# Kernel optimization log

Measured on AMD Instinct MI355X. Metric: run time of the kernel, lower is better.

## Reference

```python
import jax, jax.numpy as jnp
import numpy as np

B, TD, TE, V, D, DFF, L, H = 16, 256, 1024, 5000, 512, 2048, 6, 8

def setup_inputs():
    key = jax.random.key(0)
    ks = jax.random.split(key, 32)
    s = 0.02
    def w(k, shape):
        return jax.random.normal(k, shape, jnp.float32) * s
    # targets drawn in [3, V) so the eos filter in the torch code is a no-op
    inp = {
        "targets": jax.random.randint(ks[0], (B, TD), 3, V),
        "target_lengths": jax.random.randint(ks[1], (B,), TD // 2, TD + 1),
        "encoder_outputs": jax.random.normal(ks[2], (B, TE, D), jnp.float32),
        "encoder_output_lengths": jax.random.randint(ks[3], (B,), TE // 2, TE + 1),
        "emb": w(ks[4], (V, D)),
        "W_in": w(ks[5], (D, D)), "b_in": jnp.zeros((D,), jnp.float32),
        "ln1_g": jnp.ones((L, D), jnp.float32), "ln1_b": jnp.zeros((L, D), jnp.float32),
        "Wq1": w(ks[6], (L, D, D)), "bq1": jnp.zeros((L, D), jnp.float32),
        "Wk1": w(ks[7], (L, D, D)), "bk1": jnp.zeros((L, D), jnp.float32),
        "Wv1": w(ks[8], (L, D, D)), "bv1": jnp.zeros((L, D), jnp.float32),
        "Wo1": w(ks[9], (L, D, D)), "bo1": jnp.zeros((L, D), jnp.float32),
        "ln2_g": jnp.ones((L, D), jnp.float32), "ln2_b": jnp.zeros((L, D), jnp.float32),
        "Wq2": w(ks[10], (L, D, D)), "bq2": jnp.zeros((L, D), jnp.float32),
        "Wk2": w(ks[11], (L, D, D)), "bk2": jnp.zeros((L, D), jnp.float32),
        "Wv2": w(ks[12], (L, D, D)), "bv2": jnp.zeros((L, D), jnp.float32),
        "Wo2": w(ks[13], (L, D, D)), "bo2": jnp.zeros((L, D), jnp.float32),
        "ln3_g": jnp.ones((L, D), jnp.float32), "ln3_b": jnp.zeros((L, D), jnp.float32),
        "W_ff1": w(ks[14], (L, D, DFF)), "b_ff1": jnp.zeros((L, DFF), jnp.float32),
        "W_ff2": w(ks[15], (L, DFF, D)), "b_ff2": jnp.zeros((L, D), jnp.float32),
    }
    return inp

def _ln(x, g, b, eps=1e-5):
    m = x.mean(-1, keepdims=True)
    v = ((x - m) ** 2).mean(-1, keepdims=True)
    return (x - m) * jax.lax.rsqrt(v + eps) * g + b

def _mha(q, k, v, Wq, bq, Wk, bk, Wv, bv, Wo, bo, mask):
    Bq, Tq, Dm = q.shape
    dh = Dm // H
    def heads(x, W, bias):
        y = x @ W + bias
        return y.reshape(x.shape[0], x.shape[1], H, dh).transpose(0, 2, 1, 3)  # (B,H,T,dh)
    qh, kh, vh = heads(q, Wq, bq), heads(k, Wk, bk), heads(v, Wv, bv)
    sc = jnp.einsum('bhqd,bhkd->bhqk', qh, kh) / jnp.sqrt(jnp.float32(dh))
    sc = jnp.where(mask[:, None, :, :], jnp.float32(-1e9), sc)
    a = jax.nn.softmax(sc, axis=-1)
    ctx = jnp.einsum('bhqk,bhkd->bhqd', a, vh).transpose(0, 2, 1, 3).reshape(Bq, Tq, Dm)
    return ctx @ Wo + bo

def _pos_encoding(length, dim):
    pos = jnp.arange(length, dtype=jnp.float32)[:, None]
    div = jnp.exp(jnp.arange(0, dim, 2, dtype=jnp.float32) * (-jnp.log(jnp.float32(10000.0)) / dim))
    pe = jnp.zeros((length, dim), jnp.float32)
    pe = pe.at[:, 0::2].set(jnp.sin(pos * div)).at[:, 1::2].set(jnp.cos(pos * div))
    return pe

def _forward(targets, target_lengths, encoder_output_lengths, encoder_outputs, emb, W_in, b_in, ln1_g, ln1_b, Wq1, bq1, Wk1, bk1, Wv1, bv1, Wo1, bo1, ln2_g, ln2_b, Wq2, bq2, Wk2, bk2, Wv2, bv2, Wo2, bo2, ln3_g, ln3_b, W_ff1, b_ff1, W_ff2, b_ff2):
    Bsz, Td = targets.shape
    Te = encoder_outputs.shape[1]
    key_pad = jnp.arange(Td)[None, :] >= target_lengths[:, None]            # (B, Td) pad keys
    causal = jnp.triu(jnp.ones((Td, Td), bool), k=1)                        # subsequent mask
    self_mask = key_pad[:, None, :] | causal[None]                          # (B, Td, Td)
    enc_pad = jnp.arange(Te)[None, :] >= encoder_output_lengths[:, None]    # (B, Te)
    enc_mask = jnp.broadcast_to(enc_pad[:, None, :], (Bsz, Td, Te))
    # TransformerEmbedding: lookup * sqrt(dim), then sinusoidal PE, then input_proj
    x = emb[targets] * jnp.sqrt(jnp.float32(D)) + _pos_encoding(Td, D)[None]
    x = x @ W_in + b_in
    for l in range(L):  # pre-LN decoder layers: self-attn, cross-attn, FFN
        h = _ln(x, ln1_g[l], ln1_b[l])
        x = x + _mha(h, h, h, Wq1[l], bq1[l], Wk1[l], bk1[l], Wv1[l], bv1[l], Wo1[l], bo1[l], self_mask)
        h = _ln(x, ln2_g[l], ln2_b[l])
        x = x + _mha(h, encoder_outputs, encoder_outputs, Wq2[l], bq2[l], Wk2[l], bk2[l], Wv2[l], bv2[l], Wo2[l], bo2[l], enc_mask)
        h = _ln(x, ln3_g[l], ln3_b[l])
        x = x + (jax.nn.relu(h @ W_ff1[l] + b_ff1[l]) @ W_ff2[l] + b_ff2[l])
    # torch code stacks step_outputs[:, di, :] over di, i.e. returns the hidden states (B, Td, D)
    return x

def reference(targets, target_lengths, encoder_outputs, encoder_output_lengths, emb, W_in, b_in, ln1_g, ln1_b, Wq1, bq1, Wk1, bk1, Wv1, bv1, Wo1, bo1, ln2_g, ln2_b, Wq2, bq2, Wk2, bk2, Wv2, bv2, Wo2, bo2, ln3_g, ln3_b, W_ff1, b_ff1, W_ff2, b_ff2):
    return _forward(targets, target_lengths, encoder_output_lengths, encoder_outputs, emb, W_in, b_in, ln1_g, ln1_b, Wq1, bq1, Wk1, bk1, Wv1, bv1, Wo1, bo1, ln2_g, ln2_b, Wq2, bq2, Wk2, bk2, Wv2, bv2, Wo2, bo2, ln3_g, ln3_b, W_ff1, b_ff1, W_ff2, b_ff2)
```

## Files before the change

### kernel.cpp

```cpp
#include <hip/hip_runtime.h>
#include <hip/hip_bf16.h>

#define BB   16
#define TD   256
#define TE   1024
#define DM   512
#define DFF  2048
#define NL   6
#define NH   8
#define DH   64

typedef unsigned short u16;
typedef short short8 __attribute__((ext_vector_type(8)));
typedef float f32x4 __attribute__((ext_vector_type(4)));

__device__ __forceinline__ float b2f(u16 u) {
    unsigned int x = ((unsigned int)u) << 16;
    float f;
    __builtin_memcpy(&f, &x, 4);
    return f;
}
__device__ __forceinline__ u16 f2b(float f) {
    unsigned int x;
    __builtin_memcpy(&x, &f, 4);
    unsigned int r = x + 0x7fffu + ((x >> 16) & 1u);
    return (u16)(r >> 16);
}

__device__ __forceinline__ void gload_lds16(const u16* g, u16* l) {
    __builtin_amdgcn_global_load_lds(
        (const __attribute__((address_space(1))) unsigned int*)g,
        (__attribute__((address_space(3))) unsigned int*)l, 16, 0, 0);
}

__global__ __launch_bounds__(256) void cvt_kernel(const float* __restrict__ in,
                                                  u16* __restrict__ out, int n4) {
    int i = blockIdx.x * 256 + threadIdx.x;
    if (i < n4) {
        float4 v = reinterpret_cast<const float4*>(in)[i];
        ushort4 o;
        o.x = f2b(v.x); o.y = f2b(v.y); o.z = f2b(v.z); o.w = f2b(v.w);
        reinterpret_cast<ushort4*>(out)[i] = o;
    }
}

template <int NMAT>
struct PtrArr { const float* p[NMAT]; };

template <int NMAT>
__global__ __launch_bounds__(256) void tr_kernel(PtrArr<NMAT> P, u16* __restrict__ out,
                                                 int K, int N) {
    __shared__ u16 t[64][65];
    const float* W = P.p[blockIdx.z];
    u16* O = out + (size_t)blockIdx.z * K * N;
    int n0 = blockIdx.x * 64, k0 = blockIdx.y * 64;
    int tid = threadIdx.x;
    int r = tid >> 4, c = (tid & 15) * 4;
#pragma unroll
    for (int p = 0; p < 4; ++p) {
        int k = r + p * 16;
        float4 v = *reinterpret_cast<const float4*>(&W[(size_t)(k0 + k) * N + n0 + c]);
        t[c + 0][k] = f2b(v.x);
        t[c + 1][k] = f2b(v.y);
        t[c + 2][k] = f2b(v.z);
        t[c + 3][k] = f2b(v.w);
    }
    __syncthreads();
#pragma unroll
    for (int p = 0; p < 4; ++p) {
        int n = r + p * 16;
        ushort4 o;
        o.x = t[n][c]; o.y = t[n][c + 1]; o.z = t[n][c + 2]; o.w = t[n][c + 3];
        *reinterpret_cast<ushort4*>(&O[(size_t)(n0 + n) * K + k0 + c]) = o;
    }
}

__global__ __launch_bounds__(256) void embed_kernel(const int* __restrict__ targets,
                                                    const float* __restrict__ emb,
                                                    u16* __restrict__ out) {
    int row = blockIdx.x;
    int t   = row & (TD - 1);
    int tgt = targets[row];
    const float c = -0.017988946039015984f;
    for (int d = threadIdx.x; d < DM; d += 256) {
        float e   = emb[(size_t)tgt * DM + d] * 22.627416997969522f;
        int   i2  = d & ~1;
        float div = expf(c * (float)i2);
        float arg = (float)t * div;
        float pe  = (d & 1) ? cosf(arg) : sinf(arg);
        out[(size_t)row * DM + d] = f2b(e + pe);
    }
}

__global__ __launch_bounds__(256) void ln_kernel(const float* __restrict__ X,
                                                 const float* __restrict__ g,
                                                 const float* __restrict__ b,
                                                 size_t vo,
                                                 u16* __restrict__ O) {
    int row = blockIdx.x;
    const float* xr = X + (size_t)row * DM;
    int tid = threadIdx.x;
    float v0 = xr[tid], v1 = xr[tid + 256];
    float s = v0 + v1;
    __shared__ float red[4];
    int lane = tid & 63, wid = tid >> 6;
#pragma unroll
    for (int off = 32; off; off >>= 1) s += __shfl_xor(s, off);
    if (lane == 0) red[wid] = s;
    __syncthreads();
    float mean = (red[0] + red[1] + red[2] + red[3]) * (1.0f / 512.0f);
    float d0 = v0 - mean, d1 = v1 - mean;
    float sq = d0 * d0 + d1 * d1;
#pragma unroll
    for (int off = 32; off; off >>= 1) sq += __shfl_xor(sq, off);
    __syncthreads();
    if (lane == 0) red[wid] = sq;
    __syncthreads();
    float var = (red[0] + red[1] + red[2] + red[3]) * (1.0f / 512.0f);
    float rs  = rsqrtf(var + 1e-5f);
    O[(size_t)row * DM + tid]       = f2b(d0 * rs * g[vo + tid]       + b[vo + tid]);
    O[(size_t)row * DM + tid + 256] = f2b(d1 * rs * g[vo + tid + 256] + b[vo + tid + 256]);
}

template <int TM, int TN, bool OUTBF, bool RELU, bool RES>
__global__ __launch_bounds__(256) void gemm_bt(const u16* __restrict__ A,
                                               const u16* __restrict__ Bt,
                                               const float* __restrict__ bias, size_t bofs,
                                               const float* __restrict__ resid,
                                               void* __restrict__ C,
                                               int M, int N, int K) {
    __shared__ u16 As[2][TM * 32];
    __shared__ u16 Bs[2][TN * 32];
    int tid = threadIdx.x, wave = tid >> 6, lane = tid & 63;
    int col0 = blockIdx.x * TN, row0 = blockIdx.y * TM;
    constexpr int WM = TM / 2, WN = TN / 2;
    int wm = (wave >> 1) * WM, wn = (wave & 1) * WN;
    int lq = lane >> 4, lc = lane & 15;
    constexpr int NI = WM / 16, NJ = WN / 16;
    f32x4 acc[NI][NJ] = {};
    int srow = lane >> 2;
    int scol = (lane & 3) * 8;

    auto stage = [&](int buf, int k0) {
#pragma unroll
        for (int s = 0; s < TM / 64; ++s) {
            int rbase = wave * (TM / 4) + s * 16;
            gload_lds16(A + (size_t)(row0 + rbase + srow) * K + k0 + scol, &As[buf][rbase * 32]);
        }
#pragma unroll
        for (int s = 0; s < TN / 64; ++s) {
            int rbase = wave * (TN / 4) + s * 16;
            gload_lds16(Bt + (size_t)(col0 + rbase + srow) * K + k0 + scol, &Bs[buf][rbase * 32]);
        }
    };

    stage(0, 0);
    __syncthreads();
    int cur = 0;
    for (int k0 = 0; k0 < K; k0 += 32) {
        if (k0 + 32 < K) stage(cur ^ 1, k0 + 32);
        short8 af[NI], bf[NJ];
#pragma unroll
        for (int i = 0; i < NI; ++i)
            af[i] = *reinterpret_cast<const short8*>(&As[cur][(wm + i * 16 + lc) * 32 + lq * 8]);
#pragma unroll
        for (int j = 0; j < NJ; ++j)
            bf[j] = *reinterpret_cast<const short8*>(&Bs[cur][(wn + j * 16 + lc) * 32 + lq * 8]);
#pragma unroll
        for (int i = 0; i < NI; ++i)
#pragma unroll
            for (int j = 0; j < NJ; ++j)
                acc[i][j] = __builtin_amdgcn_mfma_f32_16x16x32_bf16(af[i], bf[j], acc[i][j], 0, 0, 0);
        __syncthreads();
        cur ^= 1;
    }

#pragma unroll
    for (int j = 0; j < NJ; ++j) {
        int n = col0 + wn + j * 16 + lc;
        float bv = bias[bofs + n];
#pragma unroll
        for (int i = 0; i < NI; ++i) {
#pragma unroll
            for (int r = 0; r < 4; ++r) {
                int m = row0 + wm + i * 16 + lq * 4 + r;
                float v = acc[i][j][r] + bv;
                if (RES)  v += resid[(size_t)m * N + n];
                if (RELU) v = fmaxf(v, 0.0f);
                if (OUTBF) ((u16*)C)[(size_t)m * N + n] = f2b(v);
                else       ((float*)C)[(size_t)m * N + n] = v;
            }
        }
    }
}

template <int NG>
struct MOut { u16* out[NG]; const float* bias[NG]; };

template <int TM, int TN, int NG>
__global__ __launch_bounds__(256) void gemm_bt_multi(const u16* __restrict__ A,
                                                     const u16* __restrict__ Bt,
                                                     MOut<NG> mo, int K) {
    __shared__ u16 As[2][TM * 32];
    __shared__ u16 Bs[2][TN * 32];
    int tid = threadIdx.x, wave = tid >> 6, lane = tid & 63;
    int col0 = blockIdx.x * TN, row0 = blockIdx.y * TM;
    constexpr int WM = TM / 2, WN = TN / 2;
    int wm = (wave >> 1) * WM, wn = (wave & 1) * WN;
    int lq = lane >> 4, lc = lane & 15;
    constexpr int NI = WM / 16, NJ = WN / 16;
    f32x4 acc[NI][NJ] = {};
    int srow = lane >> 2;
    int scol = (lane & 3) * 8;

    auto stage = [&](int buf, int k0) {
#pragma unroll
        for (int s = 0; s < TM / 64; ++s) {
            int rbase = wave * (TM / 4) + s * 16;
            gload_lds16(A + (size_t)(row0 + rbase + srow) * K + k0 + scol, &As[buf][rbase * 32]);
        }
#pragma unroll
        for (int s = 0; s < TN / 64; ++s) {
            int rbase = wave * (TN / 4) + s * 16;
            gload_lds16(Bt + (size_t)(col0 + rbase + srow) * K + k0 + scol, &Bs[buf][rbase * 32]);
        }
    };

    stage(0, 0);
    __syncthreads();
    int cur = 0;
    for (int k0 = 0; k0 < K; k0 += 32) {
        if (k0 + 32 < K) stage(cur ^ 1, k0 + 32);
        short8 af[NI], bf[NJ];
#pragma unroll
        for (int i = 0; i < NI; ++i)
            af[i] = *reinterpret_cast<const short8*>(&As[cur][(wm + i * 16 + lc) * 32 + lq * 8]);
#pragma unroll
        for (int j = 0; j < NJ; ++j)
            bf[j] = *reinterpret_cast<const short8*>(&Bs[cur][(wn + j * 16 + lc) * 32 + lq * 8]);
#pragma unroll
        for (int i = 0; i < NI; ++i)
#pragma unroll
            for (int j = 0; j < NJ; ++j)
                acc[i][j] = __builtin_amdgcn_mfma_f32_16x16x32_bf16(af[i], bf[j], acc[i][j], 0, 0, 0);
        __syncthreads();
        cur ^= 1;
    }

    int g  = col0 >> 9;
    int c0 = col0 & 511;
    u16* O = mo.out[g];
    const float* bp = mo.bias[g];
#pragma unroll
    for (int j = 0; j < NJ; ++j) {
        int n = c0 + wn + j * 16 + lc;
        float bv = bp[n];
#pragma unroll
        for (int i = 0; i < NI; ++i) {
#pragma unroll
            for (int r = 0; r < 4; ++r) {
                int m = row0 + wm + i * 16 + lq * 4 + r;
                O[(size_t)m * 512 + n] = f2b(acc[i][j][r] + bv);
            }
        }
    }
}

#define QSTR 72
#define VSTR 66

__global__ __launch_bounds__(256) void fattn_mfma(const u16* __restrict__ Q,
                                                  const u16* __restrict__ K,
                                                  const u16* __restrict__ V,
                                                  const int* __restrict__ lens,
                                                  u16* __restrict__ O,
                                                  int Tq, int Tk, int causal) {
    __shared__ u16 Qs[64 * QSTR];
    __shared__ u16 Ks[64 * QSTR];
    __shared__ u16 Ps[64 * QSTR];
    __shared__ u16 Vs[64 * VSTR];
    int tid  = threadIdx.x;
    int qt0  = blockIdx.x * 64;
    int h    = blockIdx.y;
    int b    = blockIdx.z;
    int len  = lens[b];
    int wave = tid >> 6, lane = tid & 63;
    int lq = lane >> 4, lc = lane & 15;
    int sr = tid >> 4;
    int sd = (tid & 15) * 4;

    short8 bones;
    {
        u16 v = (lc == 0) ? (u16)0x3F80 : (u16)0;
        u16 tmp[8] = { v, v, v, v, v, v, v, v };
        __builtin_memcpy(&bones, tmp, 16);
    }

#pragma unroll
    for (int i = 0; i < 4; ++i) {
        int q = sr + i * 16;
        ushort4 v = *reinterpret_cast<const ushort4*>(
            &Q[(size_t)(b * Tq + qt0 + q) * DM + h * DH + sd]);
        ushort4 w;
        w.x = f2b(b2f(v.x) * 0.125f); w.y = f2b(b2f(v.y) * 0.125f);
        w.z = f2b(b2f(v.z) * 0.125f); w.w = f2b(b2f(v.w) * 0.125f);
        *reinterpret_cast<ushort4*>(&Qs[q * QSTR + sd]) = w;
    }

    ushort4 kr[4], vr[4];
#pragma unroll
    for (int i = 0; i < 4; ++i) {
        int k = sr + i * 16;
        kr[i] = *reinterpret_cast<const ushort4*>(&K[(size_t)(b * Tk + k) * DM + h * DH + sd]);
        vr[i] = *reinterpret_cast<const ushort4*>(&V[(size_t)(b * Tk + k) * DM + h * DH + sd]);
    }
#pragma unroll
    for (int i = 0; i < 4; ++i) {
        int k = sr + i * 16;
        *reinterpret_cast<ushort4*>(&Ks[k * QSTR + sd]) = kr[i];
        Vs[(sd + 0) * VSTR + k] = vr[i].x;
        Vs[(sd + 1) * VSTR + k] = vr[i].y;
        Vs[(sd + 2) * VSTR + k] = vr[i].z;
        Vs[(sd + 3) * VSTR + k] = vr[i].w;
    }
    __syncthreads();

    short8 aq0 = *reinterpret_cast<const short8*>(&Qs[(wave * 16 + lc) * QSTR + lq * 8]);
    short8 aq1 = *reinterpret_cast<const short8*>(&Qs[(wave * 16 + lc) * QSTR + 32 + lq * 8]);

    f32x4 Ow[4] = {};
    f32x4 Ol = {};

    int kend = causal ? min(len, qt0 + 64) : len;
    for (int kt0 = 0; kt0 < kend; kt0 += 64) {
        bool more = (kt0 + 64) < kend;
        if (more) {
#pragma unroll
            for (int i = 0; i < 4; ++i) {
                int k = kt0 + 64 + sr + i * 16;
                kr[i] = *reinterpret_cast<const ushort4*>(
                    &K[(size_t)(b * Tk + k) * DM + h * DH + sd]);
                vr[i] = *reinterpret_cast<const ushort4*>(
                    &V[(size_t)(b * Tk + k) * DM + h * DH + sd]);
            }
        }

        f32x4 sa[4] = {};
#pragma unroll
        for (int n = 0; n < 4; ++n) {
            short8 bk0 = *reinterpret_cast<const short8*>(&Ks[(n * 16 + lc) * QSTR + lq * 8]);
            short8 bk1 = *reinterpret_cast<const short8*>(&Ks[(n * 16 + lc) * QSTR + 32 + lq * 8]);
            sa[n] = __builtin_amdgcn_mfma_f32_16x16x32_bf16(aq0, bk0, sa[n], 0, 0, 0);
            sa[n] = __builtin_amdgcn_mfma_f32_16x16x32_bf16(aq1, bk1, sa[n], 0, 0, 0);
        }

        int qrow_base = qt0 + wave * 16 + lq * 4;
#pragma unroll
        for (int r = 0; r < 4; ++r) {
            int qrow = qrow_base + r;
#pragma unroll
            for (int n = 0; n < 4; ++n) {
                int key = kt0 + n * 16 + lc;
                bool inv = (key >= len) || (causal && key > qrow);
                float p = inv ? 0.0f : __expf(sa[n][r] - 8.0f);
                Ps[(wave * 16 + lq * 4 + r) * QSTR + n * 16 + lc] = f2b(p);
            }
        }

        short8 ap0 = *reinterpret_cast<const short8*>(&Ps[(wave * 16 + lc) * QSTR + lq * 8]);
        short8 ap1 = *reinterpret_cast<const short8*>(&Ps[(wave * 16 + lc) * QSTR + 32 + lq * 8]);
#pragma unroll
        for (int n = 0; n < 4; ++n) {
#pragma unroll
            for (int ks = 0; ks < 2; ++ks) {
                int base = (n * 16 + lc) * VSTR + ks * 32 + lq * 8;
                const int* vp = reinterpret_cast<const int*>(&Vs[base]);
                int w[4] = { vp[0], vp[1], vp[2], vp[3] };
                short8 bv;
                __builtin_memcpy(&bv, w, 16);
                Ow[n] = __builtin_amdgcn_mfma_f32_16x16x32_bf16(ks ? ap1 : ap0, bv, Ow[n], 0, 0, 0);
            }
        }
        Ol = __builtin_amdgcn_mfma_f32_16x16x32_bf16(ap0, bones, Ol, 0, 0, 0);
        Ol = __builtin_amdgcn_mfma_f32_16x16x32_bf16(ap1, bones, Ol, 0, 0, 0);

        __syncthreads();
        if (more) {
#pragma unroll
            for (int i = 0; i < 4; ++i) {
                int k = sr + i * 16;
                *reinterpret_cast<ushort4*>(&Ks[k * QSTR + sd]) = kr[i];
                Vs[(sd + 0) * VSTR + k] = vr[i].x;
                Vs[(sd + 1) * VSTR + k] = vr[i].y;
                Vs[(sd + 2) * VSTR + k] = vr[i].z;
                Vs[(sd + 3) * VSTR + k] = vr[i].w;
            }
            __syncthreads();
        }
    }

#pragma unroll
    for (int r = 0; r < 4; ++r) {
        float lsum = __shfl(Ol[r], lane & 48);
        float inv = 1.0f / lsum;
        size_t rowoff = (size_t)(b * Tq + qt0 + wave * 16 + lq * 4 + r) * DM + h * DH;
#pragma unroll
        for (int n = 0; n < 4; ++n)
            O[rowoff + n * 16 + lc] = f2b(Ow[n][r] * inv);
    }
}

__global__ __launch_bounds__(256) void store_out_kernel(const float* __restrict__ X,
                                                        float* __restrict__ out, int n) {
    int i = blockIdx.x * 256 + threadIdx.x;
    if (i < n) out[i] = X[i];
}

extern "C" void kernel_launch(void* const* d_in, const int* in_sizes, int n_in,
                              void* d_out, int out_size, void* d_ws, size_t ws_size,
                              hipStream_t stream) {
    const int*   targets = (const int*)d_in[0];
    const int*   tlen    = (const int*)d_in[1];
    const float* enc     = (const float*)d_in[2];
    const int*   elen    = (const int*)d_in[3];
    const float* emb     = (const float*)d_in[4];
    const float* W_in    = (const float*)d_in[5];
    const float* b_in    = (const float*)d_in[6];
    const float* ln1_g   = (const float*)d_in[7];
    const float* ln1_b   = (const float*)d_in[8];
    const float* Wq1 = (const float*)d_in[9],  *bq1 = (const float*)d_in[10];
    const float* Wk1 = (const float*)d_in[11], *bk1 = (const float*)d_in[12];
    const float* Wv1 = (const float*)d_in[13], *bv1 = (const float*)d_in[14];
    const float* Wo1 = (const float*)d_in[15], *bo1 = (const float*)d_in[16];
    const float* ln2_g = (const float*)d_in[17], *ln2_b = (const float*)d_in[18];
    const float* Wq2 = (const float*)d_in[19], *bq2 = (const float*)d_in[20];
    const float* Wk2 = (const float*)d_in[21], *bk2 = (const float*)d_in[22];
    const float* Wv2 = (const float*)d_in[23], *bv2 = (const float*)d_in[24];
    const float* Wo2 = (const float*)d_in[25], *bo2 = (const float*)d_in[26];
    const float* ln3_g = (const float*)d_in[27], *ln3_b = (const float*)d_in[28];
    const float* W_ff1 = (const float*)d_in[29], *b_ff1 = (const float*)d_in[30];
    const float* W_ff2 = (const float*)d_in[31], *b_ff2 = (const float*)d_in[32];

    float* ws   = (float*)d_ws;
    float* x    = ws;
    u16*   hb   = (u16*)(ws + 2097152);
    u16*   qb   = (u16*)(ws + 3145728);
    u16*   ctx  = (u16*)(ws + 4194304);
    u16*   kb   = (u16*)(ws + 5242880);
    u16*   vb   = (u16*)(ws + 9437184);
    u16*   encb = (u16*)(ws + 13631488);
    u16*   wt_dm = (u16*)(ws + 17825792);
    u16*   wt_f1 = (u16*)(ws + 24248320);
    u16*   wt_f2 = (u16*)(ws + 27394048);
    u16*   ffh  = kb;

    PtrArr<49> pdm;
    pdm.p[0] = W_in;
    for (int l = 0; l < NL; ++l) {
        const float* ws8[8] = { Wq1, Wk1, Wv1, Wo1, Wq2, Wk2, Wv2, Wo2 };
        for (int j = 0; j < 8; ++j) pdm.p[1 + l * 8 + j] = ws8[j] + (size_t)l * DM * DM;
    }
    PtrArr<6> pf1, pf2;
    for (int l = 0; l < NL; ++l) {
        pf1.p[l] = W_ff1 + (size_t)l * DM * DFF;
        pf2.p[l] = W_ff2 + (size_t)l * DFF * DM;
    }
    tr_kernel<49><<<dim3(8, 8, 49), 256, 0, stream>>>(pdm, wt_dm, 512, 512);
    tr_kernel<6><<<dim3(32, 8, 6), 256, 0, stream>>>(pf1, wt_f1, 512, 2048);
    tr_kernel<6><<<dim3(8, 32, 6), 256, 0, stream>>>(pf2, wt_f2, 2048, 512);

    const size_t WDM = (size_t)512 * 512;
    const size_t WFF = (size_t)512 * 2048;

    const dim3 gdm(8, 64);
    const dim3 gqkv(24, 64);
    const dim3 gkv2(8, 128);
    const dim3 gf1(16, 32);
    const dim3 gattn(TD / 64, NH, BB);

    cvt_kernel<<<8192, 256, 0, stream>>>(enc, encb, BB * TE * DM / 4);
    embed_kernel<<<4096, 256, 0, stream>>>(targets, emb, hb);
    gemm_bt<64, 64, false, false, false><<<gdm, 256, 0, stream>>>(hb, wt_dm, b_in, 0, nullptr, x, 4096, 512, 512);

    for (int l = 0; l < NL; ++l) {
        const size_t vo = (size_t)l * DM;
        const size_t fv = (size_t)l * DFF;
        const u16* tq1 = wt_dm + (1 + l * 8 + 0) * WDM;
        const u16* to1 = wt_dm + (1 + l * 8 + 3) * WDM;
        const u16* tq2 = wt_dm + (1 + l * 8 + 4) * WDM;
        const u16* tk2 = wt_dm + (1 + l * 8 + 5) * WDM;
        const u16* to2 = wt_dm + (1 + l * 8 + 7) * WDM;
        const u16* tf1 = wt_f1 + l * WFF;
        const u16* tf2 = wt_f2 + l * WFF;

        ln_kernel<<<4096, 256, 0, stream>>>(x, ln1_g, ln1_b, vo, hb);
        {
            MOut<3> mo;
            mo.out[0] = qb; mo.out[1] = kb; mo.out[2] = vb;
            mo.bias[0] = bq1 + vo; mo.bias[1] = bk1 + vo; mo.bias[2] = bv1 + vo;
            gemm_bt_multi<64, 64, 3><<<gqkv, 256, 0, stream>>>(hb, tq1, mo, 512);
        }
        fattn_mfma<<<gattn, 256, 0, stream>>>(qb, kb, vb, tlen, ctx, TD, TD, 1);
        gemm_bt<64, 64, false, false, true><<<gdm, 256, 0, stream>>>(ctx, to1, bo1, vo, x, x, 4096, 512, 512);

        ln_kernel<<<4096, 256, 0, stream>>>(x, ln2_g, ln2_b, vo, hb);
        gemm_bt<64, 64, true, false, false><<<gdm, 256, 0, stream>>>(hb, tq2, bq2, vo, nullptr, qb, 4096, 512, 512);
        {
            MOut<2> mo;
            mo.out[0] = kb; mo.out[1] = vb;
            mo.bias[0] = bk2 + vo; mo.bias[1] = bv2 + vo;
            gemm_bt_multi<128, 128, 2><<<gkv2, 256, 0, stream>>>(encb, tk2, mo, 512);
        }
        fattn_mfma<<<gattn, 256, 0, stream>>>(qb, kb, vb, elen, ctx, TD, TE, 0);
        gemm_bt<64, 64, false, false, true><<<gdm, 256, 0, stream>>>(ctx, to2, bo2, vo, x, x, 4096, 512, 512);

        ln_kernel<<<4096, 256, 0, stream>>>(x, ln3_g, ln3_b, vo, hb);
        gemm_bt<128, 128, true, true, false><<<gf1, 256, 0, stream>>>(hb, tf1, b_ff1, fv, nullptr, ffh, 4096, 2048, 512);
        gemm_bt<64, 64, false, false, true><<<gdm, 256, 0, stream>>>(ffh, tf2, b_ff2, vo, x, x, 4096, 512, 2048);
    }

    store_out_kernel<<<8192, 256, 0, stream>>>(x, (float*)d_out, BB * TD * DM);
}
```

Measured before the change: 1.361 ms.

## Split cross-attention over key halves, skip padded encoder K/V rows, retile GEMMs

Cross-attention now runs as two blocks per batch, each covering half of the 1024 encoder keys. Each half writes unnormalized partial outputs and row sums, and a new combine kernel merges them. Skipping the max-subtraction with a fixed exp offset is what makes this merge valid. The encoder K/V projection skips row tiles beyond each sequence's rounded-up encoder length, and the DM-sized GEMMs move from 64x64 to 128x64 or 128x128 tiles. This buys more attention parallelism and less wasted projection work, at the cost of an extra kernel launch, partial-result memory traffic, and fewer blocks in the retiled GEMMs.

Result: slower. 1.452 ms (+6.7%).

```diff
diff --git a/kernel.cpp b/kernel.cpp
--- a/kernel.cpp
+++ b/kernel.cpp
@@ -200,11 +200,21 @@
 template <int TM, int TN, int NG>
 __global__ __launch_bounds__(256) void gemm_bt_multi(const u16* __restrict__ A,
                                                      const u16* __restrict__ Bt,
-                                                     MOut<NG> mo, int K) {
+                                                     MOut<NG> mo, int K,
+                                                     const int* __restrict__ lens,
+                                                     int rbShift) {
     __shared__ u16 As[2][TM * 32];
     __shared__ u16 Bs[2][TN * 32];
     int tid = threadIdx.x, wave = tid >> 6, lane = tid & 63;
     int col0 = blockIdx.x * TN, row0 = blockIdx.y * TM;
+
+    if (lens) {
+        int bb  = row0 >> rbShift;
+        int rl  = row0 & ((1 << rbShift) - 1);
+        int lim = (lens[bb] + 63) & ~63;
+        if (rl >= lim) return;
+    }
+
     constexpr int WM = TM / 2, WN = TN / 2;
     int wm = (wave >> 1) * WM, wn = (wave & 1) * WN;
     int lq = lane >> 4, lc = lane & 15;
@@ -269,11 +279,14 @@
 #define QSTR 72
 #define VSTR 66
 
+template <bool SPLIT>
 __global__ __launch_bounds__(256) void fattn_mfma(const u16* __restrict__ Q,
                                                   const u16* __restrict__ K,
                                                   const u16* __restrict__ V,
                                                   const int* __restrict__ lens,
                                                   u16* __restrict__ O,
+                                                  float* __restrict__ pOw,
+                                                  float* __restrict__ pl,
                                                   int Tq, int Tk, int causal) {
     __shared__ u16 Qs[64 * QSTR];
     __shared__ u16 Ks[64 * QSTR];
@@ -282,132 +295,171 @@
     int tid  = threadIdx.x;
     int qt0  = blockIdx.x * 64;
     int h    = blockIdx.y;
-    int b    = blockIdx.z;
+    int zb   = blockIdx.z;
+    int b    = SPLIT ? (zb >> 1) : zb;
+    int c    = SPLIT ? (zb & 1) : 0;
     int len  = lens[b];
     int wave = tid >> 6, lane = tid & 63;
     int lq = lane >> 4, lc = lane & 15;
     int sr = tid >> 4;
     int sd = (tid & 15) * 4;
 
-    short8 bones;
-    {
-        u16 v = (lc == 0) ? (u16)0x3F80 : (u16)0;
-        u16 tmp[8] = { v, v, v, v, v, v, v, v };
-        __builtin_memcpy(&bones, tmp, 16);
-    }
-
-#pragma unroll
-    for (int i = 0; i < 4; ++i) {
-        int q = sr + i * 16;
-        ushort4 v = *reinterpret_cast<const ushort4*>(
-            &Q[(size_t)(b * Tq + qt0 + q) * DM + h * DH + sd]);
-        ushort4 w;
-        w.x = f2b(b2f(v.x) * 0.125f); w.y = f2b(b2f(v.y) * 0.125f);
-        w.z = f2b(b2f(v.z) * 0.125f); w.w = f2b(b2f(v.w) * 0.125f);
-        *reinterpret_cast<ushort4*>(&Qs[q * QSTR + sd]) = w;
-    }
-
-    ushort4 kr[4], vr[4];
-#pragma unroll
-    for (int i = 0; i < 4; ++i) {
-        int k = sr + i * 16;
-        kr[i] = *reinterpret_cast<const ushort4*>(&K[(size_t)(b * Tk + k) * DM + h * DH + sd]);
-        vr[i] = *reinterpret_cast<const ushort4*>(&V[(size_t)(b * Tk + k) * DM + h * DH + sd]);
-    }
-#pragma unroll
-    for (int i = 0; i < 4; ++i) {
-        int k = sr + i * 16;
-        *reinterpret_cast<ushort4*>(&Ks[k * QSTR + sd]) = kr[i];
-        Vs[(sd + 0) * VSTR + k] = vr[i].x;
-        Vs[(sd + 1) * VSTR + k] = vr[i].y;
-        Vs[(sd + 2) * VSTR + k] = vr[i].z;
-        Vs[(sd + 3) * VSTR + k] = vr[i].w;
-    }
-    __syncthreads();
-
-    short8 aq0 = *reinterpret_cast<const short8*>(&Qs[(wave * 16 + lc) * QSTR + lq * 8]);
-    short8 aq1 = *reinterpret_cast<const short8*>(&Qs[(wave * 16 + lc) * QSTR + 32 + lq * 8]);
-
     f32x4 Ow[4] = {};
     f32x4 Ol = {};
 
-    int kend = causal ? min(len, qt0 + 64) : len;
-    for (int kt0 = 0; kt0 < kend; kt0 += 64) {
-        bool more = (kt0 + 64) < kend;
-        if (more) {
-#pragma unroll
-            for (int i = 0; i < 4; ++i) {
-                int k = kt0 + 64 + sr + i * 16;
-                kr[i] = *reinterpret_cast<const ushort4*>(
-                    &K[(size_t)(b * Tk + k) * DM + h * DH + sd]);
-                vr[i] = *reinterpret_cast<const ushort4*>(
-                    &V[(size_t)(b * Tk + k) * DM + h * DH + sd]);
-            }
-        }
-
-        f32x4 sa[4] = {};
-#pragma unroll
-        for (int n = 0; n < 4; ++n) {
-            short8 bk0 = *reinterpret_cast<const short8*>(&Ks[(n * 16 + lc) * QSTR + lq * 8]);
-            short8 bk1 = *reinterpret_cast<const short8*>(&Ks[(n * 16 + lc) * QSTR + 32 + lq * 8]);
-            sa[n] = __builtin_amdgcn_mfma_f32_16x16x32_bf16(aq0, bk0, sa[n], 0, 0, 0);
-            sa[n] = __builtin_amdgcn_mfma_f32_16x16x32_bf16(aq1, bk1, sa[n], 0, 0, 0);
-        }
-
-        int qrow_base = qt0 + wave * 16 + lq * 4;
+    int kend   = causal ? min(len, qt0 + 64) : len;
+    int kstart = c * 512;
+    int kcend  = SPLIT ? min(kend, kstart + 512) : kend;
+
+    if (kstart < kcend) {
+        short8 bones;
+        {
+            u16 v = (lc == 0) ? (u16)0x3F80 : (u16)0;
+            u16 tmp[8] = { v, v, v, v, v, v, v, v };
+            __builtin_memcpy(&bones, tmp, 16);
+        }
+
+#pragma unroll
+        for (int i = 0; i < 4; ++i) {
+            int q = sr + i * 16;
+            ushort4 v = *reinterpret_cast<const ushort4*>(
+                &Q[(size_t)(b * Tq + qt0 + q) * DM + h * DH + sd]);
+            ushort4 w;
+            w.x = f2b(b2f(v.x) * 0.125f); w.y = f2b(b2f(v.y) * 0.125f);
+            w.z = f2b(b2f(v.z) * 0.125f); w.w = f2b(b2f(v.w) * 0.125f);
+            *reinterpret_cast<ushort4*>(&Qs[q * QSTR + sd]) = w;
+        }
+
+        ushort4 kr[4], vr[4];
+#pragma unroll
+        for (int i = 0; i < 4; ++i) {
+            int k = kstart + sr + i * 16;
+            kr[i] = *reinterpret_cast<const ushort4*>(&K[(size_t)(b * Tk + k) * DM + h * DH + sd]);
+            vr[i] = *reinterpret_cast<const ushort4*>(&V[(size_t)(b * Tk + k) * DM + h * DH + sd]);
+        }
+#pragma unroll
+        for (int i = 0; i < 4; ++i) {
+            int k = sr + i * 16;
+            *reinterpret_cast<ushort4*>(&Ks[k * QSTR + sd]) = kr[i];
+            Vs[(sd + 0) * VSTR + k] = vr[i].x;
+            Vs[(sd + 1) * VSTR + k] = vr[i].y;
+            Vs[(sd + 2) * VSTR + k] = vr[i].z;
+            Vs[(sd + 3) * VSTR + k] = vr[i].w;
+        }
+        __syncthreads();
+
+        short8 aq0 = *reinterpret_cast<const short8*>(&Qs[(wave * 16 + lc) * QSTR + lq * 8]);
+        short8 aq1 = *reinterpret_cast<const short8*>(&Qs[(wave * 16 + lc) * QSTR + 32 + lq * 8]);
+
+        for (int kt0 = kstart; kt0 < kcend; kt0 += 64) {
+            bool more = (kt0 + 64) < kcend;
+            if (more) {
+#pragma unroll
+                for (int i = 0; i < 4; ++i) {
+                    int k = kt0 + 64 + sr + i * 16;
+                    kr[i] = *reinterpret_cast<const ushort4*>(
+                        &K[(size_t)(b * Tk + k) * DM + h * DH + sd]);
+                    vr[i] = *reinterpret_cast<const ushort4*>(
+                        &V[(size_t)(b * Tk + k) * DM + h * DH + sd]);
+                }
+            }
+
+            f32x4 sa[4] = {};
+#pragma unroll
+            for (int n = 0; n < 4; ++n) {
+                short8 bk0 = *reinterpret_cast<const short8*>(&Ks[(n * 16 + lc) * QSTR + lq * 8]);
+                short8 bk1 = *reinterpret_cast<const short8*>(&Ks[(n * 16 + lc) * QSTR + 32 + lq * 8]);
+                sa[n] = __builtin_amdgcn_mfma_f32_16x16x32_bf16(aq0, bk0, sa[n], 0, 0, 0);
+                sa[n] = __builtin_amdgcn_mfma_f32_16x16x32_bf16(aq1, bk1, sa[n], 0, 0, 0);
+            }
+
+            int qrow_base = qt0 + wave * 16 + lq * 4;
+#pragma unroll
+            for (int r = 0; r < 4; ++r) {
+                int qrow = qrow_base + r;
+#pragma unroll
+                for (int n = 0; n < 4; ++n) {
+                    int key = kt0 + n * 16 + lc;
+                    bool inv = (key >= len) || (causal && key > qrow);
+                    float p = inv ? 0.0f : __expf(sa[n][r] - 8.0f);
+                    Ps[(wave * 16 + lq * 4 + r) * QSTR + n * 16 + lc] = f2b(p);
+                }
+            }
+
+            short8 ap0 = *reinterpret_cast<const short8*>(&Ps[(wave * 16 + lc) * QSTR + lq * 8]);
+            short8 ap1 = *reinterpret_cast<const short8*>(&Ps[(wave * 16 + lc) * QSTR + 32 + lq * 8]);
+#pragma unroll
+            for (int n = 0; n < 4; ++n) {
+#pragma unroll
+                for (int ks = 0; ks < 2; ++ks) {
+                    int base = (n * 16 + lc) * VSTR + ks * 32 + lq * 8;
+                    const int* vp = reinterpret_cast<const int*>(&Vs[base]);
+                    int w[4] = { vp[0], vp[1], vp[2], vp[3] };
+                    short8 bv;
+                    __builtin_memcpy(&bv, w, 16);
+                    Ow[n] = __builtin_amdgcn_mfma_f32_16x16x32_bf16(ks ? ap1 : ap0, bv, Ow[n], 0, 0, 0);
+                }
+            }
+            Ol = __builtin_amdgcn_mfma_f32_16x16x32_bf16(ap0, bones, Ol, 0, 0, 0);
+            Ol = __builtin_amdgcn_mfma_f32_16x16x32_bf16(ap1, bones, Ol, 0, 0, 0);
+
+            __syncthreads();
+            if (more) {
+#pragma unroll
+                for (int i = 0; i < 4; ++i) {
+                    int k = sr + i * 16;
+                    *reinterpret_cast<ushort4*>(&Ks[k * QSTR + sd]) = kr[i];
+                    Vs[(sd + 0) * VSTR + k] = vr[i].x;
+                    Vs[(sd + 1) * VSTR + k] = vr[i].y;
+                    Vs[(sd + 2) * VSTR + k] = vr[i].z;
+                    Vs[(sd + 3) * VSTR + k] = vr[i].w;
+                }
+                __syncthreads();
+            }
+        }
+    }
+
+    if (SPLIT) {
+        size_t pb = ((size_t)(b * NH + h) * 2 + c) * Tq + qt0 + wave * 16 + lq * 4;
 #pragma unroll
         for (int r = 0; r < 4; ++r) {
-            int qrow = qrow_base + r;
-#pragma unroll
-            for (int n = 0; n < 4; ++n) {
-                int key = kt0 + n * 16 + lc;
-                bool inv = (key >= len) || (causal && key > qrow);
-                float p = inv ? 0.0f : __expf(sa[n][r] - 8.0f);
-                Ps[(wave * 16 + lq * 4 + r) * QSTR + n * 16 + lc] = f2b(p);
-            }
-        }
-
-        short8 ap0 = *reinterpret_cast<const short8*>(&Ps[(wave * 16 + lc) * QSTR + lq * 8]);
-        short8 ap1 = *reinterpret_cast<const short8*>(&Ps[(wave * 16 + lc) * QSTR + 32 + lq * 8]);
-#pragma unroll
-        for (int n = 0; n < 4; ++n) {
-#pragma unroll
-            for (int ks = 0; ks < 2; ++ks) {
-                int base = (n * 16 + lc) * VSTR + ks * 32 + lq * 8;
-                const int* vp = reinterpret_cast<const int*>(&Vs[base]);
-                int w[4] = { vp[0], vp[1], vp[2], vp[3] };
-                short8 bv;
-                __builtin_memcpy(&bv, w, 16);
-                Ow[n] = __builtin_amdgcn_mfma_f32_16x16x32_bf16(ks ? ap1 : ap0, bv, Ow[n], 0, 0, 0);
-            }
-        }
-        Ol = __builtin_amdgcn_mfma_f32_16x16x32_bf16(ap0, bones, Ol, 0, 0, 0);
-        Ol = __builtin_amdgcn_mfma_f32_16x16x32_bf16(ap1, bones, Ol, 0, 0, 0);
-
-        __syncthreads();
-        if (more) {
-#pragma unroll
-            for (int i = 0; i < 4; ++i) {
-                int k = sr + i * 16;
-                *reinterpret_cast<ushort4*>(&Ks[k * QSTR + sd]) = kr[i];
-                Vs[(sd + 0) * VSTR + k] = vr[i].x;
-                Vs[(sd + 1) * VSTR + k] = vr[i].y;
-                Vs[(sd + 2) * VSTR + k] = vr[i].z;
-                Vs[(sd + 3) * VSTR + k] = vr[i].w;
-            }
-            __syncthreads();
-        }
-    }
-
-#pragma unroll
-    for (int r = 0; r < 4; ++r) {
-        float lsum = __shfl(Ol[r], lane & 48);
-        float inv = 1.0f / lsum;
-        size_t rowoff = (size_t)(b * Tq + qt0 + wave * 16 + lq * 4 + r) * DM + h * DH;
-#pragma unroll
-        for (int n = 0; n < 4; ++n)
-            O[rowoff + n * 16 + lc] = f2b(Ow[n][r] * inv);
-    }
+#pragma unroll
+            for (int n = 0; n < 4; ++n)
+                pOw[(pb + r) * DH + n * 16 + lc] = Ow[n][r];
+            if (lc == 0) pl[pb + r] = Ol[r];
+        }
+    } else {
+#pragma unroll
+        for (int r = 0; r < 4; ++r) {
+            float lsum = __shfl(Ol[r], lane & 48);
+            float inv = 1.0f / lsum;
+            size_t rowoff = (size_t)(b * Tq + qt0 + wave * 16 + lq * 4 + r) * DM + h * DH;
+#pragma unroll
+            for (int n = 0; n < 4; ++n)
+                O[rowoff + n * 16 + lc] = f2b(Ow[n][r] * inv);
+        }
+    }
+}
+
+__global__ __launch_bounds__(256) void attn_combine(const float* __restrict__ pOw,
+                                                    const float* __restrict__ pl,
+                                                    u16* __restrict__ ctx) {
+    int i  = blockIdx.x * 256 + threadIdx.x;
+    int d4 = (i & 15) * 4;
+    int q  = (i >> 4) & 255;
+    int hh = (i >> 12) & 7;
+    int bb = i >> 15;
+    size_t r0 = ((size_t)(bb * NH + hh) * 2 + 0) * TD + q;
+    size_t r1 = r0 + TD;
+    float4 n0 = *reinterpret_cast<const float4*>(&pOw[r0 * DH + d4]);
+    float4 n1 = *reinterpret_cast<const float4*>(&pOw[r1 * DH + d4]);
+    float inv = 1.0f / (pl[r0] + pl[r1]);
+    ushort4 o;
+    o.x = f2b((n0.x + n1.x) * inv);
+    o.y = f2b((n0.y + n1.y) * inv);
+    o.z = f2b((n0.z + n1.z) * inv);
+    o.w = f2b((n0.w + n1.w) * inv);
+    *reinterpret_cast<ushort4*>(&ctx[((size_t)(bb * TD + q)) * DM + hh * DH + d4]) = o;
 }
 
 __global__ __launch_bounds__(256) void store_out_kernel(const float* __restrict__ X,
@@ -452,6 +504,8 @@
     u16*   wt_dm = (u16*)(ws + 17825792);
     u16*   wt_f1 = (u16*)(ws + 24248320);
     u16*   wt_f2 = (u16*)(ws + 27394048);
+    float* pOw  = ws + 30539776;
+    float* pl   = ws + 34734080;
     u16*   ffh  = kb;
 
     PtrArr<49> pdm;
@@ -472,15 +526,16 @@
     const size_t WDM = (size_t)512 * 512;
     const size_t WFF = (size_t)512 * 2048;
 
-    const dim3 gdm(8, 64);
-    const dim3 gqkv(24, 64);
+    const dim3 gop(8, 32);
+    const dim3 gqkv(12, 32);
     const dim3 gkv2(8, 128);
     const dim3 gf1(16, 32);
     const dim3 gattn(TD / 64, NH, BB);
+    const dim3 gattnX(TD / 64, NH, BB * 2);
 
     cvt_kernel<<<8192, 256, 0, stream>>>(enc, encb, BB * TE * DM / 4);
     embed_kernel<<<4096, 256, 0, stream>>>(targets, emb, hb);
-    gemm_bt<64, 64, false, false, false><<<gdm, 256, 0, stream>>>(hb, wt_dm, b_in, 0, nullptr, x, 4096, 512, 512);
+    gemm_bt<128, 64, false, false, false><<<gop, 256, 0, stream>>>(hb, wt_dm, b_in, 0, nullptr, x, 4096, 512, 512);
 
     for (int l = 0; l < NL; ++l) {
         const size_t vo = (size_t)l * DM;
@@ -498,25 +553,26 @@
             MOut<3> mo;
             mo.out[0] = qb; mo.out[1] = kb; mo.out[2] = vb;
             mo.bias[0] = bq1 + vo; mo.bias[1] = bk1 + vo; mo.bias[2] = bv1 + vo;
-            gemm_bt_multi<64, 64, 3><<<gqkv, 256, 0, stream>>>(hb, tq1, mo, 512);
-        }
-        fattn_mfma<<<gattn, 256, 0, stream>>>(qb, kb, vb, tlen, ctx, TD, TD, 1);
-        gemm_bt<64, 64, false, false, true><<<gdm, 256, 0, stream>>>(ctx, to1, bo1, vo, x, x, 4096, 512, 512);
+            gemm_bt_multi<128, 128, 3><<<gqkv, 256, 0, stream>>>(hb, tq1, mo, 512, nullptr, 0);
+        }
+        fattn_mfma<false><<<gattn, 256, 0, stream>>>(qb, kb, vb, tlen, ctx, nullptr, nullptr, TD, TD, 1);
+        gemm_bt<128, 64, false, false, true><<<gop, 256, 0, stream>>>(ctx, to1, bo1, vo, x, x, 4096, 512, 512);
 
         ln_kernel<<<4096, 256, 0, stream>>>(x, ln2_g, ln2_b, vo, hb);
-        gemm_bt<64, 64, true, false, false><<<gdm, 256, 0, stream>>>(hb, tq2, bq2, vo, nullptr, qb, 4096, 512, 512);
+        gemm_bt<128, 64, true, false, false><<<gop, 256, 0, stream>>>(hb, tq2, bq2, vo, nullptr, qb, 4096, 512, 512);
         {
             MOut<2> mo;
             mo.out[0] = kb; mo.out[1] = vb;
             mo.bias[0] = bk2 + vo; mo.bias[1] = bv2 + vo;
-            gemm_bt_multi<128, 128, 2><<<gkv2, 256, 0, stream>>>(encb, tk2, mo, 512);
-        }
-        fattn_mfma<<<gattn, 256, 0, stream>>>(qb, kb, vb, elen, ctx, TD, TE, 0);
-        gemm_bt<64, 64, false, false, true><<<gdm, 256, 0, stream>>>(ctx, to2, bo2, vo, x, x, 4096, 512, 512);
+            gemm_bt_multi<128, 128, 2><<<gkv2, 256, 0, stream>>>(encb, tk2, mo, 512, elen, 10);
+        }
+        fattn_mfma<true><<<gattnX, 256, 0, stream>>>(qb, kb, vb, elen, nullptr, pOw, pl, TD, TE, 0);
+        attn_combine<<<2048, 256, 0, stream>>>(pOw, pl, ctx);
+        gemm_bt<128, 64, false, false, true><<<gop, 256, 0, stream>>>(ctx, to2, bo2, vo, x, x, 4096, 512, 512);
 
         ln_kernel<<<4096, 256, 0, stream>>>(x, ln3_g, ln3_b, vo, hb);
         gemm_bt<128, 128, true, true, false><<<gf1, 256, 0, stream>>>(hb, tf1, b_ff1, fv, nullptr, ffh, 4096, 2048, 512);
-        gemm_bt<64, 64, false, false, true><<<gdm, 256, 0, stream>>>(ffh, tf2, b_ff2, vo, x, x, 4096, 512, 2048);
+        gemm_bt<128, 64, false, false, true><<<gop, 256, 0, stream>>>(ffh, tf2, b_ff2, vo, x, x, 4096, 512, 2048);
     }
 
     store_out_kernel<<<8192, 256, 0, stream>>>(x, (float*)d_out, BB * TD * DM);
```

## Split-K atomic residual GEMMs, skip padded encoder rows, swizzle V tile, widen QKV tile

Applied to the files above, without the earlier changes.

The residual-adding projection and FFN2 GEMMs now use split-K (2 or 4 chunks) and atomically accumulate into x, with bias added only by the first chunk. This raises block count on the small 4096x512 outputs. The cross-attention K/V projection skips 128-row tiles lying wholly beyond each batch's encoder length. The attention V tile is stored as packed key pairs in an XOR-swizzled 32-bit layout for conflict-free transposed loads, and the QKV GEMM uses a 64x128 tile. Atomics add contention and nondeterministic summation order, and skipped K/V rows leave stale buffer contents that attention must mask.

New measurement: 1.517 ms. +11.5%, slower.

```diff
diff --git a/kernel.cpp b/kernel.cpp
--- a/kernel.cpp
+++ b/kernel.cpp
@@ -11,6 +11,7 @@
 #define DH   64
 
 typedef unsigned short u16;
+typedef unsigned int u32;
 typedef short short8 __attribute__((ext_vector_type(8)));
 typedef float f32x4 __attribute__((ext_vector_type(4)));
 
@@ -122,17 +123,19 @@
     O[(size_t)row * DM + tid + 256] = f2b(d1 * rs * g[vo + tid + 256] + b[vo + tid + 256]);
 }
 
-template <int TM, int TN, bool OUTBF, bool RELU, bool RES>
+template <int TM, int TN, bool OUTBF, bool RELU, bool RES, bool ATOMIC>
 __global__ __launch_bounds__(256) void gemm_bt(const u16* __restrict__ A,
                                                const u16* __restrict__ Bt,
                                                const float* __restrict__ bias, size_t bofs,
                                                const float* __restrict__ resid,
                                                void* __restrict__ C,
-                                               int M, int N, int K) {
+                                               int M, int N, int K, int kchunk) {
     __shared__ u16 As[2][TM * 32];
     __shared__ u16 Bs[2][TN * 32];
     int tid = threadIdx.x, wave = tid >> 6, lane = tid & 63;
     int col0 = blockIdx.x * TN, row0 = blockIdx.y * TM;
+    int kbeg = blockIdx.z * kchunk;
+    int kend = kbeg + kchunk;
     constexpr int WM = TM / 2, WN = TN / 2;
     int wm = (wave >> 1) * WM, wn = (wave & 1) * WN;
     int lq = lane >> 4, lc = lane & 15;
@@ -154,11 +157,11 @@
         }
     };
 
-    stage(0, 0);
+    stage(0, kbeg);
     __syncthreads();
     int cur = 0;
-    for (int k0 = 0; k0 < K; k0 += 32) {
-        if (k0 + 32 < K) stage(cur ^ 1, k0 + 32);
+    for (int k0 = kbeg; k0 < kend; k0 += 32) {
+        if (k0 + 32 < kend) stage(cur ^ 1, k0 + 32);
         short8 af[NI], bf[NJ];
 #pragma unroll
         for (int i = 0; i < NI; ++i)
@@ -178,17 +181,21 @@
 #pragma unroll
     for (int j = 0; j < NJ; ++j) {
         int n = col0 + wn + j * 16 + lc;
-        float bv = bias[bofs + n];
+        float bv = (!ATOMIC || blockIdx.z == 0) ? bias[bofs + n] : 0.0f;
 #pragma unroll
         for (int i = 0; i < NI; ++i) {
 #pragma unroll
             for (int r = 0; r < 4; ++r) {
                 int m = row0 + wm + i * 16 + lq * 4 + r;
                 float v = acc[i][j][r] + bv;
-                if (RES)  v += resid[(size_t)m * N + n];
-                if (RELU) v = fmaxf(v, 0.0f);
-                if (OUTBF) ((u16*)C)[(size_t)m * N + n] = f2b(v);
-                else       ((float*)C)[(size_t)m * N + n] = v;
+                if (ATOMIC) {
+                    atomicAdd(&((float*)C)[(size_t)m * N + n], v);
+                } else {
+                    if (RES)  v += resid[(size_t)m * N + n];
+                    if (RELU) v = fmaxf(v, 0.0f);
+                    if (OUTBF) ((u16*)C)[(size_t)m * N + n] = f2b(v);
+                    else       ((float*)C)[(size_t)m * N + n] = v;
+                }
             }
         }
     }
@@ -200,11 +207,21 @@
 template <int TM, int TN, int NG>
 __global__ __launch_bounds__(256) void gemm_bt_multi(const u16* __restrict__ A,
                                                      const u16* __restrict__ Bt,
-                                                     MOut<NG> mo, int K) {
+                                                     MOut<NG> mo, int K,
+                                                     const int* __restrict__ lens,
+                                                     int rbShift) {
     __shared__ u16 As[2][TM * 32];
     __shared__ u16 Bs[2][TN * 32];
     int tid = threadIdx.x, wave = tid >> 6, lane = tid & 63;
     int col0 = blockIdx.x * TN, row0 = blockIdx.y * TM;
+
+    if (lens) {
+        int bb  = row0 >> rbShift;
+        int rl  = row0 & ((1 << rbShift) - 1);
+        int lim = (lens[bb] + 63) & ~63;
+        if (rl >= lim) return;
+    }
+
     constexpr int WM = TM / 2, WN = TN / 2;
     int wm = (wave >> 1) * WM, wn = (wave & 1) * WN;
     int lq = lane >> 4, lc = lane & 15;
@@ -267,7 +284,10 @@
 }
 
 #define QSTR 72
-#define VSTR 66
+
+__device__ __forceinline__ int vidx(int d, int kp) {
+    return d * 32 + (kp ^ (((d >> 2) & 7) << 2));
+}
 
 __global__ __launch_bounds__(256) void fattn_mfma(const u16* __restrict__ Q,
                                                   const u16* __restrict__ K,
@@ -278,7 +298,7 @@
     __shared__ u16 Qs[64 * QSTR];
     __shared__ u16 Ks[64 * QSTR];
     __shared__ u16 Ps[64 * QSTR];
-    __shared__ u16 Vs[64 * VSTR];
+    __shared__ u32 Vs32[64 * 32];
     int tid  = threadIdx.x;
     int qt0  = blockIdx.x * 64;
     int h    = blockIdx.y;
@@ -307,21 +327,34 @@
         *reinterpret_cast<ushort4*>(&Qs[q * QSTR + sd]) = w;
     }
 
-    ushort4 kr[4], vr[4];
+    ushort4 kr[4], vr[2][2];
 #pragma unroll
     for (int i = 0; i < 4; ++i) {
         int k = sr + i * 16;
         kr[i] = *reinterpret_cast<const ushort4*>(&K[(size_t)(b * Tk + k) * DM + h * DH + sd]);
-        vr[i] = *reinterpret_cast<const ushort4*>(&V[(size_t)(b * Tk + k) * DM + h * DH + sd]);
+    }
+#pragma unroll
+    for (int i = 0; i < 2; ++i) {
+        int kp = sr + i * 16;
+#pragma unroll
+        for (int p = 0; p < 2; ++p)
+            vr[i][p] = *reinterpret_cast<const ushort4*>(
+                &V[(size_t)(b * Tk + 2 * kp + p) * DM + h * DH + sd]);
     }
 #pragma unroll
     for (int i = 0; i < 4; ++i) {
         int k = sr + i * 16;
         *reinterpret_cast<ushort4*>(&Ks[k * QSTR + sd]) = kr[i];
-        Vs[(sd + 0) * VSTR + k] = vr[i].x;
-        Vs[(sd + 1) * VSTR + k] = vr[i].y;
-        Vs[(sd + 2) * VSTR + k] = vr[i].z;
-        Vs[(sd + 3) * VSTR + k] = vr[i].w;
+    }
+#pragma unroll
+    for (int i = 0; i < 2; ++i) {
+        int kp = sr + i * 16;
+        u16 a0[4], a1[4];
+        __builtin_memcpy(a0, &vr[i][0], 8);
+        __builtin_memcpy(a1, &vr[i][1], 8);
+#pragma unroll
+        for (int j = 0; j < 4; ++j)
+            Vs32[vidx(sd + j, kp)] = (u32)a0[j] | ((u32)a1[j] << 16);
     }
     __syncthreads();
 
@@ -340,8 +373,14 @@
                 int k = kt0 + 64 + sr + i * 16;
                 kr[i] = *reinterpret_cast<const ushort4*>(
                     &K[(size_t)(b * Tk + k) * DM + h * DH + sd]);
-                vr[i] = *reinterpret_cast<const ushort4*>(
-                    &V[(size_t)(b * Tk + k) * DM + h * DH + sd]);
+            }
+#pragma unroll
+            for (int i = 0; i < 2; ++i) {
+                int kp = sr + i * 16;
+#pragma unroll
+                for (int p = 0; p < 2; ++p)
+                    vr[i][p] = *reinterpret_cast<const ushort4*>(
+                        &V[(size_t)(b * Tk + kt0 + 64 + 2 * kp + p) * DM + h * DH + sd]);
             }
         }
 
@@ -371,13 +410,13 @@
         short8 ap1 = *reinterpret_cast<const short8*>(&Ps[(wave * 16 + lc) * QSTR + 32 + lq * 8]);
 #pragma unroll
         for (int n = 0; n < 4; ++n) {
+            int d = n * 16 + lc;
 #pragma unroll
             for (int ks = 0; ks < 2; ++ks) {
-                int base = (n * 16 + lc) * VSTR + ks * 32 + lq * 8;
-                const int* vp = reinterpret_cast<const int*>(&Vs[base]);
-                int w[4] = { vp[0], vp[1], vp[2], vp[3] };
+                int base = d * 32 + ((ks * 16 + lq * 4) ^ (((d >> 2) & 7) << 2));
+                uint4 vv = *reinterpret_cast<const uint4*>(&Vs32[base]);
                 short8 bv;
-                __builtin_memcpy(&bv, w, 16);
+                __builtin_memcpy(&bv, &vv, 16);
                 Ow[n] = __builtin_amdgcn_mfma_f32_16x16x32_bf16(ks ? ap1 : ap0, bv, Ow[n], 0, 0, 0);
             }
         }
@@ -390,10 +429,16 @@
             for (int i = 0; i < 4; ++i) {
                 int k = sr + i * 16;
                 *reinterpret_cast<ushort4*>(&Ks[k * QSTR + sd]) = kr[i];
-                Vs[(sd + 0) * VSTR + k] = vr[i].x;
-                Vs[(sd + 1) * VSTR + k] = vr[i].y;
-                Vs[(sd + 2) * VSTR + k] = vr[i].z;
-                Vs[(sd + 3) * VSTR + k] = vr[i].w;
+            }
+#pragma unroll
+            for (int i = 0; i < 2; ++i) {
+                int kp = sr + i * 16;
+                u16 a0[4], a1[4];
+                __builtin_memcpy(a0, &vr[i][0], 8);
+                __builtin_memcpy(a1, &vr[i][1], 8);
+#pragma unroll
+                for (int j = 0; j < 4; ++j)
+                    Vs32[vidx(sd + j, kp)] = (u32)a0[j] | ((u32)a1[j] << 16);
             }
             __syncthreads();
         }
@@ -473,14 +518,16 @@
     const size_t WFF = (size_t)512 * 2048;
 
     const dim3 gdm(8, 64);
-    const dim3 gqkv(24, 64);
+    const dim3 gdm2(8, 64, 2);
+    const dim3 gff2(8, 64, 4);
+    const dim3 gqkv(12, 64);
     const dim3 gkv2(8, 128);
     const dim3 gf1(16, 32);
     const dim3 gattn(TD / 64, NH, BB);
 
     cvt_kernel<<<8192, 256, 0, stream>>>(enc, encb, BB * TE * DM / 4);
     embed_kernel<<<4096, 256, 0, stream>>>(targets, emb, hb);
-    gemm_bt<64, 64, false, false, false><<<gdm, 256, 0, stream>>>(hb, wt_dm, b_in, 0, nullptr, x, 4096, 512, 512);
+    gemm_bt<64, 64, false, false, false, false><<<gdm, 256, 0, stream>>>(hb, wt_dm, b_in, 0, nullptr, x, 4096, 512, 512, 512);
 
     for (int l = 0; l < NL; ++l) {
         const size_t vo = (size_t)l * DM;
@@ -498,25 +545,25 @@
             MOut<3> mo;
             mo.out[0] = qb; mo.out[1] = kb; mo.out[2] = vb;
             mo.bias[0] = bq1 + vo; mo.bias[1] = bk1 + vo; mo.bias[2] = bv1 + vo;
-            gemm_bt_multi<64, 64, 3><<<gqkv, 256, 0, stream>>>(hb, tq1, mo, 512);
+            gemm_bt_multi<64, 128, 3><<<gqkv, 256, 0, stream>>>(hb, tq1, mo, 512, nullptr, 0);
         }
         fattn_mfma<<<gattn, 256, 0, stream>>>(qb, kb, vb, tlen, ctx, TD, TD, 1);
-        gemm_bt<64, 64, false, false, true><<<gdm, 256, 0, stream>>>(ctx, to1, bo1, vo, x, x, 4096, 512, 512);
+        gemm_bt<64, 64, false, false, false, true><<<gdm2, 256, 0, stream>>>(ctx, to1, bo1, vo, nullptr, x, 4096, 512, 512, 256);
 
         ln_kernel<<<4096, 256, 0, stream>>>(x, ln2_g, ln2_b, vo, hb);
-        gemm_bt<64, 64, true, false, false><<<gdm, 256, 0, stream>>>(hb, tq2, bq2, vo, nullptr, qb, 4096, 512, 512);
+        gemm_bt<64, 64, true, false, false, false><<<gdm, 256, 0, stream>>>(hb, tq2, bq2, vo, nullptr, qb, 4096, 512, 512, 512);
         {
             MOut<2> mo;
             mo.out[0] = kb; mo.out[1] = vb;
             mo.bias[0] = bk2 + vo; mo.bias[1] = bv2 + vo;
-            gemm_bt_multi<128, 128, 2><<<gkv2, 256, 0, stream>>>(encb, tk2, mo, 512);
+            gemm_bt_multi<128, 128, 2><<<gkv2, 256, 0, stream>>>(encb, tk2, mo, 512, elen, 10);
         }
         fattn_mfma<<<gattn, 256, 0, stream>>>(qb, kb, vb, elen, ctx, TD, TE, 0);
-        gemm_bt<64, 64, false, false, true><<<gdm, 256, 0, stream>>>(ctx, to2, bo2, vo, x, x, 4096, 512, 512);
+        gemm_bt<64, 64, false, false, false, true><<<gdm2, 256, 0, stream>>>(ctx, to2, bo2, vo, nullptr, x, 4096, 512, 512, 256);
 
         ln_kernel<<<4096, 256, 0, stream>>>(x, ln3_g, ln3_b, vo, hb);
-        gemm_bt<128, 128, true, true, false><<<gf1, 256, 0, stream>>>(hb, tf1, b_ff1, fv, nullptr, ffh, 4096, 2048, 512);
-        gemm_bt<64, 64, false, false, true><<<gdm, 256, 0, stream>>>(ffh, tf2, b_ff2, vo, x, x, 4096, 512, 2048);
+        gemm_bt<128, 128, true, true, false, false><<<gf1, 256, 0, stream>>>(hb, tf1, b_ff1, fv, nullptr, ffh, 4096, 2048, 512, 512);
+        gemm_bt<64, 64, false, false, false, true><<<gff2, 256, 0, stream>>>(ffh, tf2, b_ff2, vo, nullptr, x, 4096, 512, 2048, 512);
     }
 
     store_out_kernel<<<8192, 256, 0, stream>>>(x, (float*)d_out, BB * TD * DM);
```
